# Performance work log

Hardware: AMD Instinct MI355X
Metric: run time of the kernel (lower is better)

## Reference

```python
import jax, jax.numpy as jnp
import numpy as np

L, D = 8192, 1024


def binary_operator_diag(q_i, q_j):
    # elementwise (diagonal) linear-recurrence combine: h_j = A_j * h_i + b_j
    A_i, b_i = q_i
    A_j, b_j = q_j
    return A_j * A_i, A_j * b_i + b_j


def setup_inputs() -> dict:
    key = jax.random.key(0)
    k_in, k_u, k_th, k_bre, k_bim = jax.random.split(key, 5)
    inputs = jax.random.normal(k_in, (L, D), dtype=jnp.float32)
    # stable LRU init: |lambda| = exp(-exp(nu)) = sqrt(u), u in (0.01, 0.99)
    u = jax.random.uniform(k_u, (D,), jnp.float32, 0.01, 0.99)
    nu = jnp.log(-0.5 * jnp.log(u))
    # phase stored in log-space (forward uses exp(theta))
    theta = jnp.log(jax.random.uniform(k_th, (D,), jnp.float32, 1e-3, 6.28))
    gamma_log = 0.5 * jnp.log(1.0 - u)  # = log(sqrt(1 - |lambda|^2))
    norm = np.float32(np.sqrt(2.0 * D))
    B_re = jax.random.normal(k_bre, (D, D), jnp.float32) / norm
    B_im = jax.random.normal(k_bim, (D, D), jnp.float32) / norm
    return {"inputs": inputs, "theta": theta, "nu": nu,
            "gamma_log": gamma_log, "B_re": B_re, "B_im": B_im}


def reference(inputs, theta, nu, gamma_log, B_re, B_im):
    # diagonal transition: lambda = exp(-exp(nu) + i*exp(theta)), shape [D]
    diag_lambda = jnp.exp(-jnp.exp(nu) + 1j * jnp.exp(theta))
    # normalized input matrix: (B_re + i B_im) * exp(gamma_log)[:, None]
    B_norm = (B_re + 1j * B_im) * jnp.exp(gamma_log)[:, None]  # [D, D] complex
    # Bu[t] = B_norm @ u_t  -> batched as one GEMM: [L, D] complex
    Bu = jnp.einsum('ld,kd->lk', inputs.astype(B_norm.dtype), B_norm)
    Lambda_elements = jnp.broadcast_to(diag_lambda[None, :], Bu.shape)
    # parallel associative scan over time (axis 0), elementwise over channels
    _, hidden_states = jax.lax.associative_scan(
        binary_operator_diag, (Lambda_elements, Bu))
    return hidden_states.real + inputs
```

## Files before the change

kernel.cpp:

```cpp
#include <hip/hip_runtime.h>
#include <cstdint>
#include <cstddef>

typedef float  f32x4   __attribute__((ext_vector_type(4)));
typedef short  bf16x8  __attribute__((ext_vector_type(8)));
typedef unsigned short u16x8 __attribute__((ext_vector_type(8)));

#define L_SEQ   8192
#define D_DIM   1024
#define N_COL   2048
#define N_PAIR  512
#define CHUNK_T 16
#define N_CHUNK 512

__device__ __forceinline__ unsigned short f2bf(float f) {
  unsigned int b = __float_as_uint(f);
  b += 0x7FFFu + ((b >> 16) & 1u);
  return (unsigned short)(b >> 16);
}
__device__ __forceinline__ float bf2f(unsigned short u) {
  return __uint_as_float((unsigned int)u << 16);
}
__device__ __forceinline__ void gload_lds16(const void* g, void* lds) {
  __builtin_amdgcn_global_load_lds(
      (const __attribute__((address_space(1))) void*)g,
      (__attribute__((address_space(3))) void*)lds, 16, 0, 0);
}
__device__ __forceinline__ float2 cmul(float2 a, float2 b) {
  return make_float2(a.x * b.x - a.y * b.y, a.x * b.y + a.y * b.x);
}
__device__ __forceinline__ float2 csqr(float2 a) {
  return make_float2(a.x * a.x - a.y * a.y, 2.f * a.x * a.y);
}
__device__ __forceinline__ void cfma2(const float4& lm, float2& h0, float2& h1,
                                      const float4& v) {
  float nr0 = fmaf(lm.x, h0.x, fmaf(-lm.y, h0.y, v.x));
  float ni0 = fmaf(lm.x, h0.y, fmaf(lm.y, h0.x, v.y));
  float nr1 = fmaf(lm.z, h1.x, fmaf(-lm.w, h1.y, v.z));
  float ni1 = fmaf(lm.z, h1.y, fmaf(lm.w, h1.x, v.w));
  h0.x = nr0; h0.y = ni0; h1.x = nr1; h1.y = ni1;
}

__global__ __launch_bounds__(256) void k_prep(
    const float* __restrict__ in, const float* __restrict__ Bre,
    const float* __restrict__ Bim, const float* __restrict__ gamma_log,
    const float* __restrict__ theta, const float* __restrict__ nu,
    unsigned short* __restrict__ A, unsigned short* __restrict__ W,
    float2* __restrict__ lam) {
  int b = blockIdx.x;
  if (b < 4096) {
    int i = b * 256 + threadIdx.x;
    const float4* p = (const float4*)in;
    float4 a = p[2 * i], c = p[2 * i + 1];
    u16x8 o;
    o[0] = f2bf(a.x); o[1] = f2bf(a.y); o[2] = f2bf(a.z); o[3] = f2bf(a.w);
    o[4] = f2bf(c.x); o[5] = f2bf(c.y); o[6] = f2bf(c.z); o[7] = f2bf(c.w);
    *(u16x8*)(A + (size_t)i * 8) = o;
  } else if (b < 5120) {
    int t = (b - 4096) * 256 + threadIdx.x;
    int row = t >> 7;
    int seg = t & 127;
    int k = row >> 1;
    const float* src = (row & 1) ? Bim : Bre;
    float g = expf(gamma_log[k]);
    const float4* p = (const float4*)(src + (size_t)k * D_DIM + seg * 8);
    float4 a = p[0], c = p[1];
    u16x8 o;
    o[0] = f2bf(a.x * g); o[1] = f2bf(a.y * g); o[2] = f2bf(a.z * g); o[3] = f2bf(a.w * g);
    o[4] = f2bf(c.x * g); o[5] = f2bf(c.y * g); o[6] = f2bf(c.z * g); o[7] = f2bf(c.w * g);
    *(u16x8*)(W + (size_t)row * D_DIM + seg * 8) = o;
  } else {
    int k = (b - 5120) * 256 + threadIdx.x;
    if (k < D_DIM) {
      float mod = expf(-expf(nu[k]));
      float ang = expf(theta[k]);
      lam[k] = make_float2(mod * cosf(ang), mod * sinf(ang));
    }
  }
}

__global__ __launch_bounds__(512, 4) void k_gemm(const unsigned short* __restrict__ A,
                                                 const unsigned short* __restrict__ W,
                                                 unsigned short* __restrict__ Bu16,
                                                 float2* __restrict__ agg2,
                                                 const float2* __restrict__ lam) {
  extern __shared__ char smem[];

  const int tid = threadIdx.x;
  const int l = tid & 63, w = tid >> 6;
  const int wm = w >> 1, wn = w & 1;

  int orig = blockIdx.x;
  int wgid = (orig & 7) * 64 + (orig >> 3);
  const int mt = wgid >> 4, nt = wgid & 15;
  const size_t m0 = (size_t)mt * 256, n0 = (size_t)nt * 128;

#define STAGE_A(bb, TT) do {                                                        \
    const char* s_ = (const char*)A + m0 * 2048 + (size_t)(TT) * 64;                \
    char* d_ = smem + (bb) * 16384;                                                 \
    gload_lds16(s_ + (size_t)(tid >> 2) * 2048 + (tid & 3) * 16, d_ + tid * 16);    \
    gload_lds16(s_ + (size_t)(128 + (tid >> 2)) * 2048 + (tid & 3) * 16,            \
                d_ + 8192 + tid * 16);                                              \
  } while (0)
#define STAGE_B(bb, TT) do {                                                        \
    const char* s_ = (const char*)W + n0 * 2048 + (size_t)(TT) * 64;                \
    char* d_ = smem + 49152 + (bb) * 8192;                                          \
    gload_lds16(s_ + (size_t)(tid >> 2) * 2048 + (tid & 3) * 16, d_ + tid * 16);    \
  } while (0)

  int aoff[4], boff[4];
#pragma unroll
  for (int fr = 0; fr < 4; ++fr)
    aoff[fr] = (wm * 64 + fr * 16 + (l & 15)) * 64 + (l >> 4) * 16;
#pragma unroll
  for (int fn = 0; fn < 4; ++fn)
    boff[fn] = (wn * 64 + fn * 16 + (l & 15)) * 64 + (l >> 4) * 16;

  f32x4 acc[4][4];
#pragma unroll
  for (int m = 0; m < 4; ++m)
#pragma unroll
    for (int n = 0; n < 4; ++n) acc[m][n] = (f32x4){0.f, 0.f, 0.f, 0.f};

#define VMCNT3 asm volatile("s_waitcnt vmcnt(3)" ::: "memory")
#define VMCNT0 asm volatile("s_waitcnt vmcnt(0)" ::: "memory")
#define BAR()  do { asm volatile("" ::: "memory"); __builtin_amdgcn_s_barrier(); \
                    asm volatile("" ::: "memory"); } while (0)

  STAGE_A(0, 0); STAGE_B(0, 0);
  STAGE_A(1, 1); STAGE_B(1, 1);
  VMCNT3;
  BAR();

  for (int kt = 0; kt < 32; ++kt) {
    const int rb = kt % 3;
    if (kt + 2 < 32) {
      const int nb = (kt + 2) % 3;
      STAGE_A(nb, kt + 2);
      STAGE_B(nb, kt + 2);
    }
    const char* ab = smem + rb * 16384;
    const char* bb = smem + 49152 + rb * 8192;
    bf16x8 a_[4], b_[4];
#pragma unroll
    for (int fr = 0; fr < 4; ++fr) a_[fr] = *(const bf16x8*)(ab + aoff[fr]);
#pragma unroll
    for (int fn = 0; fn < 4; ++fn) b_[fn] = *(const bf16x8*)(bb + boff[fn]);
    __builtin_amdgcn_s_setprio(1);
#pragma unroll
    for (int fr = 0; fr < 4; ++fr)
#pragma unroll
      for (int fn = 0; fn < 4; ++fn)
        acc[fr][fn] = __builtin_amdgcn_mfma_f32_16x16x32_bf16(a_[fr], b_[fn],
                                                              acc[fr][fn], 0, 0, 0);
    __builtin_amdgcn_s_setprio(0);
    if (kt < 30) VMCNT3; else VMCNT0;
    BAR();
  }
#undef STAGE_A
#undef STAGE_B

#pragma unroll
  for (int fr = 0; fr < 4; ++fr)
#pragma unroll
    for (int fn = 0; fn < 4; ++fn) {
      int col = wn * 64 + fn * 16 + (l & 15);
#pragma unroll
      for (int j = 0; j < 4; ++j) {
        int row = wm * 64 + fr * 16 + (l >> 4) * 4 + j;
        int byte = row * 256 + ((col * 2) ^ ((row & 7) << 4));
        *(unsigned short*)(smem + byte) = f2bf(acc[fr][fn][j]);
      }
    }
  __syncthreads();

  {
    unsigned short* gbase = Bu16 + m0 * N_COL + n0;
#pragma unroll
    for (int pass = 0; pass < 8; ++pass) {
      int row = pass * 32 + (tid >> 4);
      int c = tid & 15;
      int byte = row * 256 + ((c * 16) ^ ((row & 7) << 4));
      f32x4 v = *(const f32x4*)(smem + byte);
      *(f32x4*)(gbase + (size_t)row * N_COL + c * 8) = v;
    }
  }

#pragma unroll
  for (int i = 0; i < 2; ++i) {
    int q = i * 512 + tid;
    int c = q >> 6, ch = q & 63;
    float2 lmv = lam[(n0 >> 1) + ch];
    unsigned int pr[16];
#pragma unroll
    for (int s = 0; s < 16; ++s) {
      int row = c * 16 + s;
      pr[s] = *(const unsigned int*)(smem + row * 256 + ((ch * 4) ^ ((row & 7) << 4)));
    }
    float2 h = {0.f, 0.f};
#pragma unroll
    for (int s = 0; s < 16; ++s) {
      float br = bf2f((unsigned short)(pr[s] & 0xFFFFu));
      float bi = bf2f((unsigned short)(pr[s] >> 16));
      float nr = fmaf(lmv.x, h.x, fmaf(-lmv.y, h.y, br));
      float ni = fmaf(lmv.x, h.y, fmaf(lmv.y, h.x, bi));
      h.x = nr; h.y = ni;
    }
    agg2[(size_t)(mt * 16 + c) * 1024 + (n0 >> 1) + ch] = h;
  }
}

__global__ __launch_bounds__(256) void k_scan2(const float4* __restrict__ agg4,
                                               const float4* __restrict__ lam4,
                                               float4* __restrict__ carry4) {
  int wave = blockIdx.x * 4 + (threadIdx.x >> 6);
  int lane = threadIdx.x & 63;
  int j = wave;
  float4 lm = lam4[j];
  float2 lT0 = {lm.x, lm.y}, lT1 = {lm.z, lm.w};
#pragma unroll
  for (int i = 0; i < 4; ++i) { lT0 = csqr(lT0); lT1 = csqr(lT1); }

  float4 a[8];
  float2 T0 = {0.f, 0.f}, T1 = {0.f, 0.f};
  float4 lTv = make_float4(lT0.x, lT0.y, lT1.x, lT1.y);
#pragma unroll
  for (int i = 0; i < 8; ++i) {
    a[i] = agg4[(size_t)(lane * 8 + i) * N_PAIR + j];
    cfma2(lTv, T0, T1, a[i]);
  }

  float2 M0 = lT0, M1 = lT1;
#pragma unroll
  for (int i = 0; i < 3; ++i) { M0 = csqr(M0); M1 = csqr(M1); }
  float2 S0 = T0, S1 = T1;
#pragma unroll
  for (int d = 1; d < 64; d <<= 1) {
    float2 u0, u1;
    u0.x = __shfl_up(S0.x, d); u0.y = __shfl_up(S0.y, d);
    u1.x = __shfl_up(S1.x, d); u1.y = __shfl_up(S1.y, d);
    if (lane >= d) {
      float2 m0 = cmul(M0, u0), m1 = cmul(M1, u1);
      S0.x += m0.x; S0.y += m0.y; S1.x += m1.x; S1.y += m1.y;
    }
    M0 = csqr(M0); M1 = csqr(M1);
  }
  float2 P0, P1;
  P0.x = __shfl_up(S0.x, 1); P0.y = __shfl_up(S0.y, 1);
  P1.x = __shfl_up(S1.x, 1); P1.y = __shfl_up(S1.y, 1);
  if (lane == 0) { P0 = make_float2(0.f, 0.f); P1 = make_float2(0.f, 0.f); }

#pragma unroll
  for (int i = 0; i < 8; ++i) {
    carry4[(size_t)(lane * 8 + i) * N_PAIR + j] = make_float4(P0.x, P0.y, P1.x, P1.y);
    cfma2(lTv, P0, P1, a[i]);
  }
}

__global__ __launch_bounds__(256) void k_scan3(const u16x8* __restrict__ Bu8,
                                               const float4* __restrict__ lam4,
                                               const float4* __restrict__ carry4,
                                               const ushort4* __restrict__ inA,
                                               float4* __restrict__ out4) {
  int t = blockIdx.x * 256 + threadIdx.x;
  int c = t >> 8, q = t & 255;
  float4 lm0 = lam4[2 * q], lm1 = lam4[2 * q + 1];
  float4 cv0 = carry4[(size_t)c * N_PAIR + 2 * q];
  float4 cv1 = carry4[(size_t)c * N_PAIR + 2 * q + 1];
  float2 h0 = {cv0.x, cv0.y}, h1 = {cv0.z, cv0.w};
  float2 h2 = {cv1.x, cv1.y}, h3 = {cv1.z, cv1.w};
#pragma unroll
  for (int s = 0; s < CHUNK_T; ++s) {
    size_t row = (size_t)c * CHUNK_T + s;
    u16x8 b = Bu8[row * 256 + q];
    float4 v0 = make_float4(bf2f(b[0]), bf2f(b[1]), bf2f(b[2]), bf2f(b[3]));
    float4 v1 = make_float4(bf2f(b[4]), bf2f(b[5]), bf2f(b[6]), bf2f(b[7]));
    cfma2(lm0, h0, h1, v0);
    cfma2(lm1, h2, h3, v1);
    ushort4 iv = inA[row * 256 + q];
    out4[row * 256 + q] = make_float4(h0.x + bf2f(iv.x), h1.x + bf2f(iv.y),
                                      h2.x + bf2f(iv.z), h3.x + bf2f(iv.w));
  }
}

extern "C" void kernel_launch(void* const* d_in, const int* in_sizes, int n_in,
                              void* d_out, int out_size, void* d_ws, size_t ws_size,
                              hipStream_t stream) {
  (void)in_sizes; (void)n_in; (void)out_size; (void)ws_size;
  const float* inputs    = (const float*)d_in[0];
  const float* theta     = (const float*)d_in[1];
  const float* nu        = (const float*)d_in[2];
  const float* gamma_log = (const float*)d_in[3];
  const float* Bre       = (const float*)d_in[4];
  const float* Bim       = (const float*)d_in[5];

  char* ws = (char*)d_ws;
  float2*         lam   = (float2*)ws;
  unsigned short* A     = (unsigned short*)(ws + (1 << 16));
  unsigned short* W     = (unsigned short*)(ws + (1 << 16) + (16u << 20));
  unsigned short* Bu16  = (unsigned short*)(ws + (1 << 16) + (20u << 20));
  float2*         agg   = (float2*)(ws + (1 << 16) + (52u << 20));
  float4*         carry = (float4*)(ws + (1 << 16) + (56u << 20));

  hipFuncSetAttribute((const void*)k_gemm,
                      hipFuncAttributeMaxDynamicSharedMemorySize, 73728);

  k_prep<<<5124, 256, 0, stream>>>(inputs, Bre, Bim, gamma_log, theta, nu, A, W, lam);
  k_gemm<<<512, 512, 73728, stream>>>(A, W, Bu16, agg, (const float2*)lam);
  k_scan2<<<N_PAIR / 4, 256, 0, stream>>>((const float4*)agg, (const float4*)lam, carry);
  k_scan3<<<(N_CHUNK * 256) / 256, 256, 0, stream>>>((const u16x8*)Bu16,
                                                     (const float4*)lam, carry,
                                                     (const ushort4*)A,
                                                     (float4*)d_out);
}
```

Measured before the change: 74.58 us.

## Enlarge per-wave GEMM tile to 128x64 with 4 waves and swizzled LDS staging

The GEMM workgroup drops from 8 waves to 4, so each wave now computes a 128x64 output tile with 8x4 MFMA accumulators instead of 64x64. This raises fragment reuse per LDS read and cuts the A/B LDS read traffic per MFMA. Staging loads are now issued by fewer threads (6 loads each), and an XOR swizzle on 16-byte chunks is applied to both the global-to-LDS copy and the fragment reads to reduce LDS bank conflicts. The trade-off is higher register pressure (128 accumulator registers) and fewer waves to hide latency. The epilogue and chunk-scan loops are adjusted to the smaller thread count.

```diff
diff --git a/kernel.cpp b/kernel.cpp
--- a/kernel.cpp
+++ b/kernel.cpp
@@ -79,7 +79,7 @@
   }
 }
 
-__global__ __launch_bounds__(512, 4) void k_gemm(const unsigned short* __restrict__ A,
+__global__ __launch_bounds__(256, 2) void k_gemm(const unsigned short* __restrict__ A,
                                                  const unsigned short* __restrict__ W,
                                                  unsigned short* __restrict__ Bu16,
                                                  float2* __restrict__ agg2,
@@ -95,79 +95,78 @@
   const int mt = wgid >> 4, nt = wgid & 15;
   const size_t m0 = (size_t)mt * 256, n0 = (size_t)nt * 128;
 
-#define STAGE_A(bb, TT) do {                                                        \
-    const char* s_ = (const char*)A + m0 * 2048 + (size_t)(TT) * 64;                \
-    char* d_ = smem + (bb) * 16384;                                                 \
-    gload_lds16(s_ + (size_t)(tid >> 2) * 2048 + (tid & 3) * 16, d_ + tid * 16);    \
-    gload_lds16(s_ + (size_t)(128 + (tid >> 2)) * 2048 + (tid & 3) * 16,            \
-                d_ + 8192 + tid * 16);                                              \
+  const int sch = (tid & 3) ^ ((tid >> 3) & 3);
+  const size_t soff = (size_t)(tid >> 2) * 2048 + (size_t)sch * 16;
+
+#define STAGE(bb, TT) do {                                                          \
+    const char* sa = (const char*)A + m0 * 2048 + (size_t)(TT) * 64;                \
+    char* da = smem + (bb) * 16384;                                                 \
+    gload_lds16(sa + soff,          da + tid * 16);                                 \
+    gload_lds16(sa + 131072 + soff, da + 4096 + tid * 16);                          \
+    gload_lds16(sa + 262144 + soff, da + 8192 + tid * 16);                          \
+    gload_lds16(sa + 393216 + soff, da + 12288 + tid * 16);                         \
+    const char* sb = (const char*)W + n0 * 2048 + (size_t)(TT) * 64;                \
+    char* db = smem + 49152 + (bb) * 8192;                                          \
+    gload_lds16(sb + soff,          db + tid * 16);                                 \
+    gload_lds16(sb + 131072 + soff, db + 4096 + tid * 16);                          \
   } while (0)
-#define STAGE_B(bb, TT) do {                                                        \
-    const char* s_ = (const char*)W + n0 * 2048 + (size_t)(TT) * 64;                \
-    char* d_ = smem + 49152 + (bb) * 8192;                                          \
-    gload_lds16(s_ + (size_t)(tid >> 2) * 2048 + (tid & 3) * 16, d_ + tid * 16);    \
-  } while (0)
-
-  int aoff[4], boff[4];
-#pragma unroll
-  for (int fr = 0; fr < 4; ++fr)
-    aoff[fr] = (wm * 64 + fr * 16 + (l & 15)) * 64 + (l >> 4) * 16;
+
+  const int swk = (((l >> 4)) ^ ((l >> 1) & 3)) << 4;
+  int aoff[8], boff[4];
+#pragma unroll
+  for (int fr = 0; fr < 8; ++fr)
+    aoff[fr] = (wm * 128 + fr * 16 + (l & 15)) * 64 + swk;
 #pragma unroll
   for (int fn = 0; fn < 4; ++fn)
-    boff[fn] = (wn * 64 + fn * 16 + (l & 15)) * 64 + (l >> 4) * 16;
-
-  f32x4 acc[4][4];
-#pragma unroll
-  for (int m = 0; m < 4; ++m)
+    boff[fn] = (wn * 64 + fn * 16 + (l & 15)) * 64 + swk;
+
+  f32x4 acc[8][4];
+#pragma unroll
+  for (int m = 0; m < 8; ++m)
 #pragma unroll
     for (int n = 0; n < 4; ++n) acc[m][n] = (f32x4){0.f, 0.f, 0.f, 0.f};
 
-#define VMCNT3 asm volatile("s_waitcnt vmcnt(3)" ::: "memory")
+#define VMCNT6 asm volatile("s_waitcnt vmcnt(6)" ::: "memory")
 #define VMCNT0 asm volatile("s_waitcnt vmcnt(0)" ::: "memory")
 #define BAR()  do { asm volatile("" ::: "memory"); __builtin_amdgcn_s_barrier(); \
                     asm volatile("" ::: "memory"); } while (0)
 
-  STAGE_A(0, 0); STAGE_B(0, 0);
-  STAGE_A(1, 1); STAGE_B(1, 1);
-  VMCNT3;
+  STAGE(0, 0);
+  STAGE(1, 1);
+  VMCNT6;
   BAR();
 
   for (int kt = 0; kt < 32; ++kt) {
     const int rb = kt % 3;
-    if (kt + 2 < 32) {
-      const int nb = (kt + 2) % 3;
-      STAGE_A(nb, kt + 2);
-      STAGE_B(nb, kt + 2);
-    }
+    if (kt + 2 < 32) STAGE((kt + 2) % 3, kt + 2);
     const char* ab = smem + rb * 16384;
     const char* bb = smem + 49152 + rb * 8192;
-    bf16x8 a_[4], b_[4];
-#pragma unroll
-    for (int fr = 0; fr < 4; ++fr) a_[fr] = *(const bf16x8*)(ab + aoff[fr]);
+    bf16x8 a_[8], b_[4];
+#pragma unroll
+    for (int fr = 0; fr < 8; ++fr) a_[fr] = *(const bf16x8*)(ab + aoff[fr]);
 #pragma unroll
     for (int fn = 0; fn < 4; ++fn) b_[fn] = *(const bf16x8*)(bb + boff[fn]);
     __builtin_amdgcn_s_setprio(1);
 #pragma unroll
-    for (int fr = 0; fr < 4; ++fr)
+    for (int fr = 0; fr < 8; ++fr)
 #pragma unroll
       for (int fn = 0; fn < 4; ++fn)
         acc[fr][fn] = __builtin_amdgcn_mfma_f32_16x16x32_bf16(a_[fr], b_[fn],
                                                               acc[fr][fn], 0, 0, 0);
     __builtin_amdgcn_s_setprio(0);
-    if (kt < 30) VMCNT3; else VMCNT0;
+    if (kt < 30) VMCNT6; else VMCNT0;
     BAR();
   }
-#undef STAGE_A
-#undef STAGE_B
-
-#pragma unroll
-  for (int fr = 0; fr < 4; ++fr)
+#undef STAGE
+
+#pragma unroll
+  for (int fr = 0; fr < 8; ++fr)
 #pragma unroll
     for (int fn = 0; fn < 4; ++fn) {
       int col = wn * 64 + fn * 16 + (l & 15);
 #pragma unroll
       for (int j = 0; j < 4; ++j) {
-        int row = wm * 64 + fr * 16 + (l >> 4) * 4 + j;
+        int row = wm * 128 + fr * 16 + (l >> 4) * 4 + j;
         int byte = row * 256 + ((col * 2) ^ ((row & 7) << 4));
         *(unsigned short*)(smem + byte) = f2bf(acc[fr][fn][j]);
       }
@@ -177,8 +176,8 @@
   {
     unsigned short* gbase = Bu16 + m0 * N_COL + n0;
 #pragma unroll
-    for (int pass = 0; pass < 8; ++pass) {
-      int row = pass * 32 + (tid >> 4);
+    for (int pass = 0; pass < 16; ++pass) {
+      int row = pass * 16 + (tid >> 4);
       int c = tid & 15;
       int byte = row * 256 + ((c * 16) ^ ((row & 7) << 4));
       f32x4 v = *(const f32x4*)(smem + byte);
@@ -187,8 +186,8 @@
   }
 
 #pragma unroll
-  for (int i = 0; i < 2; ++i) {
-    int q = i * 512 + tid;
+  for (int i = 0; i < 4; ++i) {
+    int q = i * 256 + tid;
     int c = q >> 6, ch = q & 63;
     float2 lmv = lam[(n0 >> 1) + ch];
     unsigned int pr[16];
@@ -306,7 +305,7 @@
                       hipFuncAttributeMaxDynamicSharedMemorySize, 73728);
 
   k_prep<<<5124, 256, 0, stream>>>(inputs, Bre, Bim, gamma_log, theta, nu, A, W, lam);
-  k_gemm<<<512, 512, 73728, stream>>>(A, W, Bu16, agg, (const float2*)lam);
+  k_gemm<<<512, 256, 73728, stream>>>(A, W, Bu16, agg, (const float2*)lam);
   k_scan2<<<N_PAIR / 4, 256, 0, stream>>>((const float4*)agg, (const float4*)lam, carry);
   k_scan3<<<(N_CHUNK * 256) / 256, 256, 0, stream>>>((const u16x8*)Bu16,
                                                      (const float4*)lam, carry,
```

New measurement: 73.71 us. Within noise of the previous version (-1.2%).
